# Optimization experiments

Hardware: AMD Instinct MI355X
Metric: run time of the kernel (lower is better)

Reference implementation:

```python
import jax, jax.numpy as jnp
import numpy as np

BETA = 10.0    # ste surrogate-gradient scale (module default beta=10)
SLOPE = 1.0
GAMMA = 100.0  # trigger sharpness (module default gamma=100)
EPS = 1e-30

# Straight-through estimator: hard threshold forward, sigmoid-derivative surrogate backward
@jax.custom_vjp
def ste(v):
    return (v > 0).astype(v.dtype)

def _ste_fwd(v):
    return ste(v), v

def _ste_bwd(v, g):
    e = jnp.exp(-SLOPE * v)
    return (BETA * g * SLOPE * e / ((e + 1.0) ** 2 + EPS),)

ste.defvjp(_ste_fwd, _ste_bwd)


def setup_inputs() -> dict:
    key = jax.random.key(0)
    k1, k2, k3 = jax.random.split(key, 3)
    B, I, O = 256, 1024, 1024
    ACT_RATIO = 0.1
    x = jax.random.normal(k1, (B, I), dtype=jnp.float32)
    v_weight = jax.random.uniform(k2, (O, I), dtype=jnp.float32) - (1.0 - ACT_RATIO)
    # fc weight: xavier uniform
    bound = float(np.sqrt(6.0 / (I + O)))
    fc_weight = jax.random.uniform(k3, (O, I), dtype=jnp.float32, minval=-bound, maxval=bound)
    return {"x": x, "v_weight": v_weight, "fc_weight": fc_weight}


def reference(x, v_weight, fc_weight):
    # x: [B, I]; v_weight, fc_weight: [O, I]
    mask = ste(v_weight)                        # [O, I], 0/1 child mask
    x_en = x[:, None, :] * mask                 # [B, O, I] (x_enlarge * ste(v))
    w = fc_weight * mask                        # [O, I] masked matmul weight
    y = x @ w.T                                 # [B, O]
    # trigger value: tanh(gamma*|x|) where child, 1 where not; prod over input dim
    delta_en = jnp.tanh(GAMMA * jnp.abs(x_en)) * mask + (1.0 - mask)  # [B, O, I]
    delta = jnp.prod(delta_en, axis=-1)         # [B, O]
    y = jax.nn.relu(y * delta)
    return (y, delta)
```

## Files before the change

kernel.cpp:

```cpp
#include <hip/hip_runtime.h>
#include <cmath>

#define B_ 256
#define I_ 1024
#define O_ 1024

typedef __attribute__((ext_vector_type(8))) short short8;
typedef __attribute__((ext_vector_type(4))) float f32x4;

__device__ inline unsigned f2bf(float f) {
  union { float f; unsigned u; } c;
  c.f = f;
  unsigned u = c.u;
  return (u + 0x7FFFu + ((u >> 16) & 1u)) >> 16;
}

__device__ inline float fast_lt(float xv) {
  float z = 100.0f * fabsf(xv);
  float t = __expf(-2.0f * z);
  float lt = __logf((1.0f - t) / (1.0f + t));
  return fmaxf(lt, -1e30f);
}

__global__ __launch_bounds__(512) void prep2(
    const float* __restrict__ x, const float* __restrict__ vw,
    const float* __restrict__ fcw, unsigned short* __restrict__ xb,
    unsigned short* __restrict__ ltb, unsigned short* __restrict__ wb) {
  const int t = threadIdx.x;
  const int bid = blockIdx.x;
  {
    size_t idx = ((size_t)bid * 512 + t) * 8;
    float4 v0 = *reinterpret_cast<const float4*>(vw + idx);
    float4 v1 = *reinterpret_cast<const float4*>(vw + idx + 4);
    float4 f0 = *reinterpret_cast<const float4*>(fcw + idx);
    float4 f1 = *reinterpret_cast<const float4*>(fcw + idx + 4);
    float va[8] = {v0.x, v0.y, v0.z, v0.w, v1.x, v1.y, v1.z, v1.w};
    float fa[8] = {f0.x, f0.y, f0.z, f0.w, f1.x, f1.y, f1.z, f1.w};
    short8 wv;
#pragma unroll
    for (int j = 0; j < 8; ++j)
      wv[j] = (va[j] > 0.0f) ? (short)f2bf(fa[j]) : (short)0;
    *reinterpret_cast<short8*>(wb + idx) = wv;
  }
  if (t < 128) {
    size_t idx = ((size_t)bid * 128 + t) * 8;
    float4 x0 = *reinterpret_cast<const float4*>(x + idx);
    float4 x1 = *reinterpret_cast<const float4*>(x + idx + 4);
    float xa[8] = {x0.x, x0.y, x0.z, x0.w, x1.x, x1.y, x1.z, x1.w};
    short8 xv, lv;
#pragma unroll
    for (int j = 0; j < 8; ++j) {
      xv[j] = (short)f2bf(xa[j]);
      lv[j] = (short)f2bf(fast_lt(xa[j]));
    }
    *reinterpret_cast<short8*>(xb + idx) = xv;
    *reinterpret_cast<short8*>(ltb + idx) = lv;
  }
}

__global__ __launch_bounds__(512) void mfma_fused5(
    const unsigned short* __restrict__ xb, const unsigned short* __restrict__ ltb,
    const unsigned short* __restrict__ wb, float* __restrict__ out) {
  const int bid = blockIdx.x;
  const int cx = bid & 7;
  const int wi = bid >> 3;
  const int nblk = cx * 4 + (wi >> 3);
  const int mblk = wi & 7;
  const int on0 = nblk * 32;
  const int bm0 = mblk * 32;

  __shared__ short As[2][32][72];
  __shared__ short Ls[2][32][72];
  __shared__ short Ws[2][32][72];
  __shared__ short Ms[2][32][72];

  const int t = threadIdx.x;
  const int lane = t & 63;
  const int wid = t >> 6;
  const int kg = wid >> 2;
  const int wm = (wid >> 1) & 1, wn = wid & 1;
  const int lr = lane & 15;
  const int lk = (lane >> 4) * 8;

  const int tl = t & 255;
  const int srow = tl >> 3;
  const int scol = (tl & 7) * 8;

  const size_t aoff = (size_t)(bm0 + srow) * I_ + kg * 512 + scol;
  const size_t boff = (size_t)(on0 + srow) * I_ + kg * 512 + scol;

  short8 rx = *reinterpret_cast<const short8*>(xb + aoff);
  short8 rl = *reinterpret_cast<const short8*>(ltb + aoff);
  short8 rw = *reinterpret_cast<const short8*>(wb + boff);

  f32x4 accd = {0.f, 0.f, 0.f, 0.f};
  f32x4 accs = {0.f, 0.f, 0.f, 0.f};

  for (int kt = 0; kt < 512; kt += 64) {
    short8 rm;
#pragma unroll
    for (int j = 0; j < 8; ++j)
      rm[j] = rw[j] ? (short)0x3F80 : (short)0;
    __syncthreads();
    *reinterpret_cast<short8*>(&As[kg][srow][scol]) = rx;
    *reinterpret_cast<short8*>(&Ls[kg][srow][scol]) = rl;
    *reinterpret_cast<short8*>(&Ws[kg][srow][scol]) = rw;
    *reinterpret_cast<short8*>(&Ms[kg][srow][scol]) = rm;
    if (kt + 64 < 512) {
      rx = *reinterpret_cast<const short8*>(xb + aoff + kt + 64);
      rl = *reinterpret_cast<const short8*>(ltb + aoff + kt + 64);
      rw = *reinterpret_cast<const short8*>(wb + boff + kt + 64);
    }
    __syncthreads();
#pragma unroll
    for (int ks = 0; ks < 2; ++ks) {
      const int kb = ks * 32 + lk;
      short8 af = *reinterpret_cast<const short8*>(&As[kg][wm * 16 + lr][kb]);
      short8 lf = *reinterpret_cast<const short8*>(&Ls[kg][wm * 16 + lr][kb]);
      short8 wf = *reinterpret_cast<const short8*>(&Ws[kg][wn * 16 + lr][kb]);
      short8 mf = *reinterpret_cast<const short8*>(&Ms[kg][wn * 16 + lr][kb]);
      accd = __builtin_amdgcn_mfma_f32_16x16x32_bf16(af, wf, accd, 0, 0, 0);
      accs = __builtin_amdgcn_mfma_f32_16x16x32_bf16(lf, mf, accs, 0, 0, 0);
    }
  }

  __syncthreads();
  float* red = reinterpret_cast<float*>(&As[0][0][0]);
  const int ridx = ((wid & 3) * 64 + lane) * 8;
  if (kg == 1) {
#pragma unroll
    for (int r = 0; r < 4; ++r) {
      red[ridx + r] = accd[r];
      red[ridx + 4 + r] = accs[r];
    }
  }
  __syncthreads();
  if (kg == 0) {
    const int orow = bm0 + wm * 16 + (lane >> 4) * 4;
    const int ocol = on0 + wn * 16 + lr;
#pragma unroll
    for (int r = 0; r < 4; ++r) {
      float dsum = accd[r] + red[ridx + r];
      float ssum = accs[r] + red[ridx + 4 + r];
      float d = __expf(ssum);
      float y = fmaxf(dsum * d, 0.0f);
      size_t off = (size_t)(orow + r) * O_ + ocol;
      out[off] = y;
      out[(size_t)B_ * O_ + off] = d;
    }
  }
}

__global__ __launch_bounds__(256) void dual_gemm_f32(
    const float* __restrict__ x, const float* __restrict__ vw,
    const float* __restrict__ fcw, float* __restrict__ out) {
  const int on0 = blockIdx.x * 64;
  const int bm0 = blockIdx.y * 64;
  __shared__ float xs[32][68];
  __shared__ float ls[32][68];
  __shared__ float wsm[32][68];
  __shared__ float msh[32][68];
  const int t = threadIdx.x;
  const int tx = t & 15, ty = t >> 4;
  const int m0 = ty * 4, n0 = tx * 4;
  float accd[4][4] = {{0.f}};
  float accs[4][4] = {{0.f}};
  for (int kt = 0; kt < I_; kt += 32) {
#pragma unroll
    for (int j = 0; j < 8; ++j) {
      int f = j * 256 + t;
      int m = f >> 5;
      int kk = f & 31;
      int gk = kt + kk;
      float xv = x[(size_t)(bm0 + m) * I_ + gk];
      xs[kk][m] = xv;
      ls[kk][m] = fast_lt(xv);
      float vv = vw[(size_t)(on0 + m) * I_ + gk];
      float fv = fcw[(size_t)(on0 + m) * I_ + gk];
      float mk = vv > 0.0f ? 1.0f : 0.0f;
      wsm[kk][m] = fv * mk;
      msh[kk][m] = mk;
    }
    __syncthreads();
#pragma unroll
    for (int kk = 0; kk < 32; ++kk) {
      float4 xv = *reinterpret_cast<const float4*>(&xs[kk][m0]);
      float4 lv = *reinterpret_cast<const float4*>(&ls[kk][m0]);
      float4 wv = *reinterpret_cast<const float4*>(&wsm[kk][n0]);
      float4 mv = *reinterpret_cast<const float4*>(&msh[kk][n0]);
      float xa[4] = {xv.x, xv.y, xv.z, xv.w};
      float la[4] = {lv.x, lv.y, lv.z, lv.w};
      float wa[4] = {wv.x, wv.y, wv.z, wv.w};
      float ma[4] = {mv.x, mv.y, mv.z, mv.w};
#pragma unroll
      for (int i = 0; i < 4; ++i)
#pragma unroll
        for (int jj = 0; jj < 4; ++jj) {
          accd[i][jj] = fmaf(xa[i], wa[jj], accd[i][jj]);
          accs[i][jj] = fmaf(la[i], ma[jj], accs[i][jj]);
        }
    }
    __syncthreads();
  }
#pragma unroll
  for (int i = 0; i < 4; ++i) {
    int row = bm0 + m0 + i;
#pragma unroll
    for (int jj = 0; jj < 4; ++jj) {
      float delta = __expf(accs[i][jj]);
      out[(size_t)row * O_ + on0 + n0 + jj] = fmaxf(accd[i][jj] * delta, 0.0f);
      out[(size_t)B_ * O_ + (size_t)row * O_ + on0 + n0 + jj] = delta;
    }
  }
}

extern "C" void kernel_launch(void* const* d_in, const int* in_sizes, int n_in,
                              void* d_out, int out_size, void* d_ws,
                              size_t ws_size, hipStream_t stream) {
  const float* x = (const float*)d_in[0];
  const float* vw = (const float*)d_in[1];
  const float* fcw = (const float*)d_in[2];
  float* out = (float*)d_out;

  const size_t xbB = (size_t)B_ * I_ * 2;
  const size_t wbB = (size_t)O_ * I_ * 2;
  const size_t needB = 2 * xbB + wbB;

  unsigned short* xb = (unsigned short*)d_ws;
  unsigned short* ltb = (unsigned short*)((char*)d_ws + xbB);
  unsigned short* wb = (unsigned short*)((char*)d_ws + 2 * xbB);

  if (ws_size >= needB) {
    prep2<<<256, 512, 0, stream>>>(x, vw, fcw, xb, ltb, wb);
    mfma_fused5<<<256, 512, 0, stream>>>(xb, ltb, wb, out);
  } else {
    dual_gemm_f32<<<dim3(O_ / 64, B_ / 64, 1), 256, 0, stream>>>(x, vw, fcw, out);
  }
}
```

Measured before the change: 17.14 us.

## Split K four ways and derive mask from weight tile at fragment time

New measurement: 16.30 us. 4.9% less time.

```diff
diff --git a/kernel.cpp b/kernel.cpp
--- a/kernel.cpp
+++ b/kernel.cpp
@@ -58,7 +58,7 @@
   }
 }
 
-__global__ __launch_bounds__(512) void mfma_fused5(
+__global__ __launch_bounds__(512) void mfma_fused6(
     const unsigned short* __restrict__ xb, const unsigned short* __restrict__ ltb,
     const unsigned short* __restrict__ wb, float* __restrict__ out) {
   const int bid = blockIdx.x;
@@ -69,84 +69,108 @@
   const int on0 = nblk * 32;
   const int bm0 = mblk * 32;
 
-  __shared__ short As[2][32][72];
-  __shared__ short Ls[2][32][72];
-  __shared__ short Ws[2][32][72];
-  __shared__ short Ms[2][32][72];
+  __shared__ short lds[4][3][32][72];
 
   const int t = threadIdx.x;
   const int lane = t & 63;
   const int wid = t >> 6;
-  const int kg = wid >> 2;
-  const int wm = (wid >> 1) & 1, wn = wid & 1;
+  const int kg = wid >> 1;
+  const int w2 = wid & 1;
   const int lr = lane & 15;
   const int lk = (lane >> 4) * 8;
 
-  const int tl = t & 255;
-  const int srow = tl >> 3;
-  const int scol = (tl & 7) * 8;
-
-  const size_t aoff = (size_t)(bm0 + srow) * I_ + kg * 512 + scol;
-  const size_t boff = (size_t)(on0 + srow) * I_ + kg * 512 + scol;
-
-  short8 rx = *reinterpret_cast<const short8*>(xb + aoff);
-  short8 rl = *reinterpret_cast<const short8*>(ltb + aoff);
-  short8 rw = *reinterpret_cast<const short8*>(wb + boff);
-
-  f32x4 accd = {0.f, 0.f, 0.f, 0.f};
-  f32x4 accs = {0.f, 0.f, 0.f, 0.f};
-
-  for (int kt = 0; kt < 512; kt += 64) {
-    short8 rm;
-#pragma unroll
-    for (int j = 0; j < 8; ++j)
-      rm[j] = rw[j] ? (short)0x3F80 : (short)0;
-    __syncthreads();
-    *reinterpret_cast<short8*>(&As[kg][srow][scol]) = rx;
-    *reinterpret_cast<short8*>(&Ls[kg][srow][scol]) = rl;
-    *reinterpret_cast<short8*>(&Ws[kg][srow][scol]) = rw;
-    *reinterpret_cast<short8*>(&Ms[kg][srow][scol]) = rm;
-    if (kt + 64 < 512) {
-      rx = *reinterpret_cast<const short8*>(xb + aoff + kt + 64);
-      rl = *reinterpret_cast<const short8*>(ltb + aoff + kt + 64);
-      rw = *reinterpret_cast<const short8*>(wb + boff + kt + 64);
+  const int tl = t & 127;
+  const int srow = tl >> 2;
+  const int scol = (tl & 3) * 16;
+
+  const size_t aoff = (size_t)(bm0 + srow) * I_ + kg * 256 + scol;
+  const size_t boff = (size_t)(on0 + srow) * I_ + kg * 256 + scol;
+
+  short8 rx0 = *reinterpret_cast<const short8*>(xb + aoff);
+  short8 rx1 = *reinterpret_cast<const short8*>(xb + aoff + 8);
+  short8 rl0 = *reinterpret_cast<const short8*>(ltb + aoff);
+  short8 rl1 = *reinterpret_cast<const short8*>(ltb + aoff + 8);
+  short8 rw0 = *reinterpret_cast<const short8*>(wb + boff);
+  short8 rw1 = *reinterpret_cast<const short8*>(wb + boff + 8);
+
+  f32x4 z = {0.f, 0.f, 0.f, 0.f};
+  f32x4 accd0 = z, accd1 = z, accs0 = z, accs1 = z;
+
+  for (int kt = 0; kt < 256; kt += 64) {
+    __syncthreads();
+    *reinterpret_cast<short8*>(&lds[kg][0][srow][scol]) = rx0;
+    *reinterpret_cast<short8*>(&lds[kg][0][srow][scol + 8]) = rx1;
+    *reinterpret_cast<short8*>(&lds[kg][1][srow][scol]) = rl0;
+    *reinterpret_cast<short8*>(&lds[kg][1][srow][scol + 8]) = rl1;
+    *reinterpret_cast<short8*>(&lds[kg][2][srow][scol]) = rw0;
+    *reinterpret_cast<short8*>(&lds[kg][2][srow][scol + 8]) = rw1;
+    if (kt + 64 < 256) {
+      rx0 = *reinterpret_cast<const short8*>(xb + aoff + kt + 64);
+      rx1 = *reinterpret_cast<const short8*>(xb + aoff + kt + 72);
+      rl0 = *reinterpret_cast<const short8*>(ltb + aoff + kt + 64);
+      rl1 = *reinterpret_cast<const short8*>(ltb + aoff + kt + 72);
+      rw0 = *reinterpret_cast<const short8*>(wb + boff + kt + 64);
+      rw1 = *reinterpret_cast<const short8*>(wb + boff + kt + 72);
     }
     __syncthreads();
 #pragma unroll
     for (int ks = 0; ks < 2; ++ks) {
       const int kb = ks * 32 + lk;
-      short8 af = *reinterpret_cast<const short8*>(&As[kg][wm * 16 + lr][kb]);
-      short8 lf = *reinterpret_cast<const short8*>(&Ls[kg][wm * 16 + lr][kb]);
-      short8 wf = *reinterpret_cast<const short8*>(&Ws[kg][wn * 16 + lr][kb]);
-      short8 mf = *reinterpret_cast<const short8*>(&Ms[kg][wn * 16 + lr][kb]);
-      accd = __builtin_amdgcn_mfma_f32_16x16x32_bf16(af, wf, accd, 0, 0, 0);
-      accs = __builtin_amdgcn_mfma_f32_16x16x32_bf16(lf, mf, accs, 0, 0, 0);
+      short8 af = *reinterpret_cast<const short8*>(&lds[kg][0][w2 * 16 + lr][kb]);
+      short8 lf = *reinterpret_cast<const short8*>(&lds[kg][1][w2 * 16 + lr][kb]);
+      short8 wf0 = *reinterpret_cast<const short8*>(&lds[kg][2][lr][kb]);
+      short8 wf1 = *reinterpret_cast<const short8*>(&lds[kg][2][16 + lr][kb]);
+      short8 mf0, mf1;
+#pragma unroll
+      for (int j = 0; j < 8; ++j) {
+        mf0[j] = wf0[j] ? (short)0x3F80 : (short)0;
+        mf1[j] = wf1[j] ? (short)0x3F80 : (short)0;
+      }
+      accd0 = __builtin_amdgcn_mfma_f32_16x16x32_bf16(af, wf0, accd0, 0, 0, 0);
+      accd1 = __builtin_amdgcn_mfma_f32_16x16x32_bf16(af, wf1, accd1, 0, 0, 0);
+      accs0 = __builtin_amdgcn_mfma_f32_16x16x32_bf16(lf, mf0, accs0, 0, 0, 0);
+      accs1 = __builtin_amdgcn_mfma_f32_16x16x32_bf16(lf, mf1, accs1, 0, 0, 0);
     }
   }
 
   __syncthreads();
-  float* red = reinterpret_cast<float*>(&As[0][0][0]);
-  const int ridx = ((wid & 3) * 64 + lane) * 8;
-  if (kg == 1) {
+  float* red = reinterpret_cast<float*>(&lds[0][0][0][0]);
+  if (kg > 0) {
+    float* p = red + (((kg - 1) * 128 + w2 * 64 + lane) << 4);
 #pragma unroll
     for (int r = 0; r < 4; ++r) {
-      red[ridx + r] = accd[r];
-      red[ridx + 4 + r] = accs[r];
+      p[r] = accd0[r];
+      p[4 + r] = accd1[r];
+      p[8 + r] = accs0[r];
+      p[12 + r] = accs1[r];
     }
   }
   __syncthreads();
   if (kg == 0) {
-    const int orow = bm0 + wm * 16 + (lane >> 4) * 4;
-    const int ocol = on0 + wn * 16 + lr;
+#pragma unroll
+    for (int g = 0; g < 3; ++g) {
+      const float* p = red + ((g * 128 + w2 * 64 + lane) << 4);
+#pragma unroll
+      for (int r = 0; r < 4; ++r) {
+        accd0[r] += p[r];
+        accd1[r] += p[4 + r];
+        accs0[r] += p[8 + r];
+        accs1[r] += p[12 + r];
+      }
+    }
+    const int orow = bm0 + w2 * 16 + (lane >> 4) * 4;
+    const int ocol = on0 + lr;
 #pragma unroll
     for (int r = 0; r < 4; ++r) {
-      float dsum = accd[r] + red[ridx + r];
-      float ssum = accs[r] + red[ridx + 4 + r];
-      float d = __expf(ssum);
-      float y = fmaxf(dsum * d, 0.0f);
-      size_t off = (size_t)(orow + r) * O_ + ocol;
-      out[off] = y;
-      out[(size_t)B_ * O_ + off] = d;
+      float d0 = __expf(accs0[r]);
+      float d1 = __expf(accs1[r]);
+      float y0 = fmaxf(accd0[r] * d0, 0.0f);
+      float y1 = fmaxf(accd1[r] * d1, 0.0f);
+      size_t off0 = (size_t)(orow + r) * O_ + ocol;
+      out[off0] = y0;
+      out[off0 + 16] = y1;
+      out[(size_t)B_ * O_ + off0] = d0;
+      out[(size_t)B_ * O_ + off0 + 16] = d1;
     }
   }
 }
@@ -232,7 +256,7 @@
 
   if (ws_size >= needB) {
     prep2<<<256, 512, 0, stream>>>(x, vw, fcw, xb, ltb, wb);
-    mfma_fused5<<<256, 512, 0, stream>>>(xb, ltb, wb, out);
+    mfma_fused6<<<256, 512, 0, stream>>>(xb, ltb, wb, out);
   } else {
     dual_gemm_f32<<<dim3(O_ / 64, B_ / 64, 1), 256, 0, stream>>>(x, vw, fcw, out);
   }
```

## Split GEMM tiles to 16x32 with 4-way K split and in-register mask

Applied to the files above, without the earlier changes.

Result: faster. 16.31 us (-4.8%).

```diff
diff --git a/kernel.cpp b/kernel.cpp
--- a/kernel.cpp
+++ b/kernel.cpp
@@ -58,92 +58,99 @@
   }
 }
 
-__global__ __launch_bounds__(512) void mfma_fused5(
+__global__ __launch_bounds__(512, 4) void mfma_fused8(
     const unsigned short* __restrict__ xb, const unsigned short* __restrict__ ltb,
     const unsigned short* __restrict__ wb, float* __restrict__ out) {
   const int bid = blockIdx.x;
   const int cx = bid & 7;
   const int wi = bid >> 3;
-  const int nblk = cx * 4 + (wi >> 3);
-  const int mblk = wi & 7;
+  const int nblk = cx * 4 + (wi >> 4);
+  const int mblk = wi & 15;
   const int on0 = nblk * 32;
-  const int bm0 = mblk * 32;
-
-  __shared__ short As[2][32][72];
-  __shared__ short Ls[2][32][72];
-  __shared__ short Ws[2][32][72];
-  __shared__ short Ms[2][32][72];
+  const int bm0 = mblk * 16;
+
+  __shared__ short lds[4][64][72];
 
   const int t = threadIdx.x;
   const int lane = t & 63;
   const int wid = t >> 6;
-  const int kg = wid >> 2;
-  const int wm = (wid >> 1) & 1, wn = wid & 1;
+  const int kg = wid >> 1;
+  const int w2 = wid & 1;
   const int lr = lane & 15;
   const int lk = (lane >> 4) * 8;
 
-  const int tl = t & 255;
-  const int srow = tl >> 3;
-  const int scol = (tl & 7) * 8;
-
-  const size_t aoff = (size_t)(bm0 + srow) * I_ + kg * 512 + scol;
-  const size_t boff = (size_t)(on0 + srow) * I_ + kg * 512 + scol;
-
-  short8 rx = *reinterpret_cast<const short8*>(xb + aoff);
-  short8 rl = *reinterpret_cast<const short8*>(ltb + aoff);
-  short8 rw = *reinterpret_cast<const short8*>(wb + boff);
+  const int tl = t & 127;
+  const int ar = tl >> 3;
+  const int ac = (tl & 7) * 8;
+  const int wr = tl >> 2;
+  const int wc = (tl & 3) * 16;
+
+  const size_t aoff = (size_t)(bm0 + ar) * I_ + kg * 256 + ac;
+  const size_t boff = (size_t)(on0 + wr) * I_ + kg * 256 + wc;
+
+  short8 ra = *reinterpret_cast<const short8*>(xb + aoff);
+  short8 rlv = *reinterpret_cast<const short8*>(ltb + aoff);
+  short8 rw0 = *reinterpret_cast<const short8*>(wb + boff);
+  short8 rw1 = *reinterpret_cast<const short8*>(wb + boff + 8);
 
   f32x4 accd = {0.f, 0.f, 0.f, 0.f};
   f32x4 accs = {0.f, 0.f, 0.f, 0.f};
 
-  for (int kt = 0; kt < 512; kt += 64) {
-    short8 rm;
-#pragma unroll
-    for (int j = 0; j < 8; ++j)
-      rm[j] = rw[j] ? (short)0x3F80 : (short)0;
-    __syncthreads();
-    *reinterpret_cast<short8*>(&As[kg][srow][scol]) = rx;
-    *reinterpret_cast<short8*>(&Ls[kg][srow][scol]) = rl;
-    *reinterpret_cast<short8*>(&Ws[kg][srow][scol]) = rw;
-    *reinterpret_cast<short8*>(&Ms[kg][srow][scol]) = rm;
-    if (kt + 64 < 512) {
-      rx = *reinterpret_cast<const short8*>(xb + aoff + kt + 64);
-      rl = *reinterpret_cast<const short8*>(ltb + aoff + kt + 64);
-      rw = *reinterpret_cast<const short8*>(wb + boff + kt + 64);
+  for (int kt = 0; kt < 256; kt += 64) {
+    __syncthreads();
+    *reinterpret_cast<short8*>(&lds[kg][ar][ac]) = ra;
+    *reinterpret_cast<short8*>(&lds[kg][16 + ar][ac]) = rlv;
+    *reinterpret_cast<short8*>(&lds[kg][32 + wr][wc]) = rw0;
+    *reinterpret_cast<short8*>(&lds[kg][32 + wr][wc + 8]) = rw1;
+    if (kt + 64 < 256) {
+      ra = *reinterpret_cast<const short8*>(xb + aoff + kt + 64);
+      rlv = *reinterpret_cast<const short8*>(ltb + aoff + kt + 64);
+      rw0 = *reinterpret_cast<const short8*>(wb + boff + kt + 64);
+      rw1 = *reinterpret_cast<const short8*>(wb + boff + kt + 72);
     }
     __syncthreads();
 #pragma unroll
     for (int ks = 0; ks < 2; ++ks) {
       const int kb = ks * 32 + lk;
-      short8 af = *reinterpret_cast<const short8*>(&As[kg][wm * 16 + lr][kb]);
-      short8 lf = *reinterpret_cast<const short8*>(&Ls[kg][wm * 16 + lr][kb]);
-      short8 wf = *reinterpret_cast<const short8*>(&Ws[kg][wn * 16 + lr][kb]);
-      short8 mf = *reinterpret_cast<const short8*>(&Ms[kg][wn * 16 + lr][kb]);
+      short8 af = *reinterpret_cast<const short8*>(&lds[kg][lr][kb]);
+      short8 lf = *reinterpret_cast<const short8*>(&lds[kg][16 + lr][kb]);
+      short8 wf = *reinterpret_cast<const short8*>(&lds[kg][32 + w2 * 16 + lr][kb]);
+      short8 mf;
+#pragma unroll
+      for (int j = 0; j < 8; ++j)
+        mf[j] = wf[j] ? (short)0x3F80 : (short)0;
       accd = __builtin_amdgcn_mfma_f32_16x16x32_bf16(af, wf, accd, 0, 0, 0);
       accs = __builtin_amdgcn_mfma_f32_16x16x32_bf16(lf, mf, accs, 0, 0, 0);
     }
   }
 
   __syncthreads();
-  float* red = reinterpret_cast<float*>(&As[0][0][0]);
-  const int ridx = ((wid & 3) * 64 + lane) * 8;
-  if (kg == 1) {
+  float* red = reinterpret_cast<float*>(&lds[0][0][0]);
+  if (kg > 0) {
+    float* p = red + (((kg - 1) * 128 + w2 * 64 + lane) << 3);
 #pragma unroll
     for (int r = 0; r < 4; ++r) {
-      red[ridx + r] = accd[r];
-      red[ridx + 4 + r] = accs[r];
+      p[r] = accd[r];
+      p[4 + r] = accs[r];
     }
   }
   __syncthreads();
   if (kg == 0) {
-    const int orow = bm0 + wm * 16 + (lane >> 4) * 4;
-    const int ocol = on0 + wn * 16 + lr;
+#pragma unroll
+    for (int g = 0; g < 3; ++g) {
+      const float* p = red + ((g * 128 + w2 * 64 + lane) << 3);
+#pragma unroll
+      for (int r = 0; r < 4; ++r) {
+        accd[r] += p[r];
+        accs[r] += p[4 + r];
+      }
+    }
+    const int orow = bm0 + (lane >> 4) * 4;
+    const int ocol = on0 + w2 * 16 + lr;
 #pragma unroll
     for (int r = 0; r < 4; ++r) {
-      float dsum = accd[r] + red[ridx + r];
-      float ssum = accs[r] + red[ridx + 4 + r];
-      float d = __expf(ssum);
-      float y = fmaxf(dsum * d, 0.0f);
+      float d = __expf(accs[r]);
+      float y = fmaxf(accd[r] * d, 0.0f);
       size_t off = (size_t)(orow + r) * O_ + ocol;
       out[off] = y;
       out[(size_t)B_ * O_ + off] = d;
@@ -232,7 +239,7 @@
 
   if (ws_size >= needB) {
     prep2<<<256, 512, 0, stream>>>(x, vw, fcw, xb, ltb, wb);
-    mfma_fused5<<<256, 512, 0, stream>>>(xb, ltb, wb, out);
+    mfma_fused8<<<512, 512, 0, stream>>>(xb, ltb, wb, out);
   } else {
     dual_gemm_f32<<<dim3(O_ / 64, B_ / 64, 1), 256, 0, stream>>>(x, vw, fcw, out);
   }
```
